# Kernel optimization log

Measured on AMD Instinct MI355X. Metric: run time of the kernel, lower is better.

Reference implementation:

```python
import jax, jax.numpy as jnp
import numpy as np

N_NODES = 50000
N_EDGES = 800000
IN_DIM, HID_DIM, OUT_DIM = 128, 128, 64


def setup_inputs() -> dict:
    key = jax.random.key(0)
    ks = jax.random.split(key, 8)
    x = jax.random.normal(ks[0], (N_NODES, IN_DIM), dtype=jnp.float32)
    edge_index = jax.random.randint(ks[1], (2, N_EDGES), 0, N_NODES, dtype=jnp.int64)
    # GCNConv uses Glorot weights + zero bias; any random init is fine for a reference
    W1 = jax.random.normal(ks[2], (IN_DIM, HID_DIM), dtype=jnp.float32) / np.sqrt(IN_DIM)
    b1 = jnp.zeros((HID_DIM,), dtype=jnp.float32)
    W2 = jax.random.normal(ks[3], (HID_DIM, OUT_DIM), dtype=jnp.float32) / np.sqrt(HID_DIM)
    b2 = jnp.zeros((OUT_DIM,), dtype=jnp.float32)
    Wfc = jax.random.normal(ks[4], (OUT_DIM, 2), dtype=jnp.float32) / np.sqrt(OUT_DIM)
    bfc = jnp.zeros((2,), dtype=jnp.float32)
    return {"x": x, "edge_index": edge_index, "W1": W1, "b1": b1,
            "W2": W2, "b2": b2, "Wfc": Wfc, "bfc": bfc}


def _gcn_conv(x, src, dst, W, b, n_nodes):
    """PyG GCNConv: out = D^{-1/2} (A+I) D^{-1/2} (x W) + b."""
    xw = x @ W  # [N, F_out] transform before propagation
    ones = jnp.ones(src.shape[0], dtype=xw.dtype)
    deg = jax.ops.segment_sum(ones, dst, num_segments=n_nodes) + 1.0  # +1 for self-loop
    dinv = jax.lax.rsqrt(deg)
    norm = dinv[src] * dinv[dst]  # [E]
    msg = xw[src] * norm[:, None]  # gather + scale: [E, F_out]
    agg = jax.ops.segment_sum(msg, dst, num_segments=n_nodes)  # scatter-add
    agg = agg + xw * (dinv * dinv)[:, None]  # self-loop contribution (norm = 1/deg)
    return agg + b


def reference(x, edge_index, W1, b1, W2, b2, Wfc, bfc):
    n = x.shape[0]
    src, dst = edge_index[0], edge_index[1]
    h = jax.nn.relu(_gcn_conv(x, src, dst, W1, b1, n))
    # dropout is identity in eval mode
    h = _gcn_conv(h, src, dst, W2, b2, n)
    h = h @ Wfc + bfc
    return jax.nn.leaky_relu(h, negative_slope=0.01)
```

## Files before the change

kernel.cpp:

```cpp
#include <hip/hip_runtime.h>
#include <hip/hip_fp16.h>

#define IN_DIM 128
#define HID_DIM 128
#define OUT_DIM 64
#define BINW 128
#define BINSHIFT 7
#define MAXBIN 512
#define CAP 4096
#define CNTSTRIDE 16
#define SC_GRID 256
#define SBUF 3456

typedef _Float16 f16x8 __attribute__((ext_vector_type(8)));
typedef float f32x4 __attribute__((ext_vector_type(4)));

__global__ __launch_bounds__(256) void k_build_gemm(const float* __restrict__ x,
                                                    const float* __restrict__ W,
                                                    __half* __restrict__ xwh,
                                                    const int* __restrict__ src,
                                                    const int* __restrict__ dst,
                                                    int* __restrict__ bin_cnt,
                                                    int* __restrict__ ovf_cnt,
                                                    unsigned int* __restrict__ ovf,
                                                    unsigned int* __restrict__ ebin,
                                                    int N, int E, int nbin) {
    __shared__ union SMem {
        unsigned int wt_raw[8192];
        struct {
            int h[MAXBIN];
            int excl[MAXBIN];
            int base_s[MAXBIN];
            int ps[256];
            unsigned int sortbuf[SBUF];
        } sc;
    } smem;
    const int nGemm = (N + 127) >> 7;
    int tid = threadIdx.x;

    if ((int)blockIdx.x < nGemm) {
        char* wb = (char*)smem.wt_raw;
        {
            int kk0 = (tid & 15) * 2;
            int c8  = (tid >> 4) * 8;
#pragma unroll
            for (int i = 0; i < 4; ++i) {
                int kk = i * 32 + kk0;
                const float* w0 = W + (size_t)kk * HID_DIM + c8;
                const float* w1 = w0 + HID_DIM;
                float4 a0 = *(const float4*)w0;
                float4 a1 = *(const float4*)(w0 + 4);
                float4 b0 = *(const float4*)w1;
                float4 b1 = *(const float4*)(w1 + 4);
                float va[8] = {a0.x, a0.y, a0.z, a0.w, a1.x, a1.y, a1.z, a1.w};
                float vb[8] = {b0.x, b0.y, b0.z, b0.w, b1.x, b1.y, b1.z, b1.w};
#pragma unroll
                for (int j = 0; j < 8; ++j) {
                    int col = c8 + j;
                    int byte = (col << 8) + (kk << 1);
                    byte ^= ((col & 7) << 4);
                    *(__half2*)(wb + byte) = __floats2half2_rn(va[j], vb[j]);
                }
            }
        }
        int lane = tid & 63;
        int wv   = tid >> 6;
        int lcol = lane & 15;
        int lk   = (lane >> 4) << 3;
        int swz  = (lcol & 7) << 4;
        int rb   = blockIdx.x * 128 + wv * 32;
        int rows[2];
        const float* xp[2];
#pragma unroll
        for (int r = 0; r < 2; ++r) {
            int row = rb + 16 * r + lcol;
            rows[r] = row;
            if (row > N - 1) row = N - 1;
            xp[r] = x + (size_t)row * IN_DIM + lk;
        }
        f32x4 acc[2][8];
#pragma unroll
        for (int r = 0; r < 2; ++r)
#pragma unroll
            for (int c = 0; c < 8; ++c) acc[r][c] = (f32x4){0.f, 0.f, 0.f, 0.f};

        __syncthreads();

        auto mk = [](float4 f0, float4 f1, f16x8& hi, f16x8& lo) {
            float f[8] = {f0.x, f0.y, f0.z, f0.w, f1.x, f1.y, f1.z, f1.w};
#pragma unroll
            for (int e = 0; e < 8; ++e) {
                _Float16 h = (_Float16)f[e];
                hi[e] = h;
                lo[e] = (_Float16)(f[e] - (float)h);
            }
        };
#pragma unroll
        for (int kc = 0; kc < 4; ++kc) {
            f16x8 xhi[2], xlo[2];
#pragma unroll
            for (int r = 0; r < 2; ++r) {
                float4 f0 = *(const float4*)(xp[r] + kc * 32);
                float4 f1 = *(const float4*)(xp[r] + kc * 32 + 4);
                mk(f0, f1, xhi[r], xlo[r]);
            }
#pragma unroll
            for (int c = 0; c < 8; ++c) {
                int ad = ((c << 12) | (lcol << 8) | ((kc << 6) + (lk << 1))) ^ swz;
                f16x8 wfrag = *(const f16x8*)(wb + ad);
                acc[0][c] = __builtin_amdgcn_mfma_f32_16x16x32_f16(wfrag, xhi[0], acc[0][c], 0, 0, 0);
                acc[0][c] = __builtin_amdgcn_mfma_f32_16x16x32_f16(wfrag, xlo[0], acc[0][c], 0, 0, 0);
                acc[1][c] = __builtin_amdgcn_mfma_f32_16x16x32_f16(wfrag, xhi[1], acc[1][c], 0, 0, 0);
                acc[1][c] = __builtin_amdgcn_mfma_f32_16x16x32_f16(wfrag, xlo[1], acc[1][c], 0, 0, 0);
            }
        }
        int cq = lane >> 4;
#pragma unroll
        for (int r = 0; r < 2; ++r) {
            if (rows[r] < N) {
                uint2* p = (uint2*)(xwh + (size_t)rows[r] * HID_DIM);
#pragma unroll
                for (int c = 0; c < 8; ++c) {
                    union { __half2 h[2]; uint2 u; } pk;
                    pk.h[0] = __floats2half2_rn(acc[r][c].x, acc[r][c].y);
                    pk.h[1] = __floats2half2_rn(acc[r][c].z, acc[r][c].w);
                    p[4 * c + cq] = pk.u;
                }
            }
        }
    } else {
        int sb = blockIdx.x - nGemm;
        int* h = smem.sc.h;
        int* excl = smem.sc.excl;
        int* base_s = smem.sc.base_s;
        int* ps = smem.sc.ps;
        unsigned int* sortbuf = smem.sc.sortbuf;
        for (int k = tid; k < MAXBIN; k += 256) h[k] = 0;
        __syncthreads();
        int per = E / SC_GRID;
        int ebeg = sb * per;
        int eend = (sb + 1 == SC_GRID) ? E : ebeg + per;
        for (int i = ebeg + tid; i < eend; i += 256)
            atomicAdd(&h[dst[i] >> BINSHIFT], 1);
        __syncthreads();
        int b0 = 2 * tid, b1 = 2 * tid + 1;
        int c0 = h[b0], c1 = h[b1];
        ps[tid] = c0 + c1;
        __syncthreads();
        for (int off = 1; off < 256; off <<= 1) {
            int v = (tid >= off) ? ps[tid - off] : 0;
            __syncthreads();
            ps[tid] += v;
            __syncthreads();
        }
        int Pprev = (tid > 0) ? ps[tid - 1] : 0;
        excl[b0] = Pprev;
        excl[b1] = Pprev + c0;
        __syncthreads();
        for (int k = tid; k < nbin; k += 256) {
            int c = h[k];
            base_s[k] = (c > 0) ? atomicAdd(&bin_cnt[k * CNTSTRIDE], c) : 0;
            h[k] = 0;
        }
        __syncthreads();
        for (int i = ebeg + tid; i < eend; i += 256) {
            unsigned int s = (unsigned int)src[i];
            unsigned int d = (unsigned int)dst[i];
            int b = (int)(d >> BINSHIFT);
            int r = atomicAdd(&h[b], 1);
            sortbuf[excl[b] + r] = s | (d << 16);
        }
        __syncthreads();
        int tot = eend - ebeg;
        for (int i = tid; i < tot; i += 256) {
            unsigned int p = sortbuf[i];
            int b = (int)(p >> (16 + BINSHIFT));
            int g = base_s[b] + (i - excl[b]);
            if (g < CAP) ebin[(size_t)b * CAP + g] = p;
            else ovf[atomicAdd(ovf_cnt, 1)] = p;
        }
    }
}

__global__ __launch_bounds__(256) void k_fill(const unsigned int* __restrict__ ebin,
                                              const int* __restrict__ bin_cnt,
                                              const int* __restrict__ ovf_cnt,
                                              const unsigned int* __restrict__ ovf,
                                              int* __restrict__ row_ptr,
                                              unsigned short* __restrict__ degu,
                                              unsigned short* __restrict__ csr_src,
                                              float* __restrict__ dinv,
                                              const float* __restrict__ W2,
                                              const float* __restrict__ Wfc,
                                              const float* __restrict__ b2,
                                              const float* __restrict__ bfc,
                                              float* __restrict__ Wc,
                                              float* __restrict__ bc,
                                              int N, int nbin) {
    __shared__ int cnt[BINW];
    __shared__ int excl[BINW];
    __shared__ int start[BINW];
    int k = blockIdx.x;
    int node0 = k * BINW;
    int nn = min(BINW, N - node0);
    int t = threadIdx.x;
    if (t < BINW) cnt[t] = 0;
    __syncthreads();
    int cnt_k = min(bin_cnt[k * CNTSTRIDE], CAP);
    const unsigned int* seg = ebin + (size_t)k * CAP;
    for (int i = t; i < cnt_k; i += 256)
        atomicAdd(&cnt[(seg[i] >> 16) & (BINW - 1)], 1);
    int novf = *ovf_cnt;
    for (int i = t; i < novf; i += 256) {
        unsigned int e = ovf[i];
        if ((int)(e >> (16 + BINSHIFT)) == k)
            atomicAdd(&cnt[(e >> 16) & (BINW - 1)], 1);
    }
    __syncthreads();
    if (t < BINW) excl[t] = (t < nn) ? cnt[t] : 0;
    __syncthreads();
    for (int off = 1; off < BINW; off <<= 1) {
        int u = 0;
        if (t < BINW && t >= off) u = excl[t - off];
        __syncthreads();
        if (t < BINW) excl[t] += u;
        __syncthreads();
    }
    if (t < nn) {
        int deg = cnt[t];
        int e0 = k * CAP + excl[t] - deg;
        start[t] = e0;
        row_ptr[node0 + t] = e0;
        degu[node0 + t] = (unsigned short)deg;
        dinv[node0 + t] = rsqrtf((float)deg + 1.0f);
        cnt[t] = 0;
    }
    __syncthreads();
    for (int i = t; i < cnt_k; i += 256) {
        unsigned int e = seg[i];
        int dl = (e >> 16) & (BINW - 1);
        int slot = start[dl] + atomicAdd(&cnt[dl], 1);
        csr_src[slot] = (unsigned short)(e & 0xffffu);
    }
    for (int i = t; i < novf; i += 256) {
        unsigned int e = ovf[i];
        if ((int)(e >> (16 + BINSHIFT)) == k) {
            int dl = (e >> 16) & (BINW - 1);
            int slot = start[dl] + atomicAdd(&cnt[dl], 1);
            csr_src[slot] = (unsigned short)(e & 0xffffu);
        }
    }
    if (k == 0) {
        int kk = t >> 1, j = t & 1;
        float acc = 0.f;
#pragma unroll 8
        for (int m = 0; m < OUT_DIM; ++m) acc += W2[kk * OUT_DIM + m] * Wfc[m * 2 + j];
        Wc[kk * 2 + j] = acc;
        if (kk == 0) {
            float b = 0.f;
#pragma unroll 8
            for (int m = 0; m < OUT_DIM; ++m) b += b2[m] * Wfc[m * 2 + j];
            bc[j] = b + bfc[j];
        }
    }
}

__global__ __launch_bounds__(256) void k_agg1z(const int* __restrict__ row_ptr,
                                               const unsigned short* __restrict__ degu,
                                               const unsigned short* __restrict__ csr_src,
                                               const float* __restrict__ dinv,
                                               const __half* __restrict__ xwh,
                                               const float* __restrict__ b1,
                                               const float* __restrict__ Wc,
                                               float* __restrict__ z, int N) {
    constexpr int F = HID_DIM;
    constexpr int L = F / 8;
    constexpr int EPW = 64 / L;
    __shared__ float Wcs[HID_DIM * 2];
    int tid = threadIdx.x;
    if (tid < 64) ((float4*)Wcs)[tid] = ((const float4*)Wc)[tid];
    __syncthreads();
    int node = (blockIdx.x * 256 + tid) >> 6;
    if (node >= N) return;
    int lane = tid & 63;
    int sub = lane / L;
    int c   = lane % L;
    int beg = row_ptr[node];
    int end = beg + degu[node];
    float dd = dinv[node];
    uint4 us = *(const uint4*)(xwh + (size_t)node * F + c * 8);
    float4 b1a = *(const float4*)(b1 + c * 8);
    float4 b1b = *(const float4*)(b1 + c * 8 + 4);
    float a0 = 0.f, a1 = 0.f, a2 = 0.f, a3 = 0.f;
    float a4 = 0.f, a5 = 0.f, a6 = 0.f, a7 = 0.f;
    auto acc = [&](uint4 u, float w) {
        float2 v0 = __half22float2(*(__half2*)&u.x);
        float2 v1 = __half22float2(*(__half2*)&u.y);
        float2 v2 = __half22float2(*(__half2*)&u.z);
        float2 v3 = __half22float2(*(__half2*)&u.w);
        a0 = fmaf(v0.x, w, a0); a1 = fmaf(v0.y, w, a1);
        a2 = fmaf(v1.x, w, a2); a3 = fmaf(v1.y, w, a3);
        a4 = fmaf(v2.x, w, a4); a5 = fmaf(v2.y, w, a5);
        a6 = fmaf(v3.x, w, a6); a7 = fmaf(v3.y, w, a7);
    };
    int j = beg + sub;
    for (; j + 3 * EPW < end; j += 4 * EPW) {
        int s0 = csr_src[j];
        int s1 = csr_src[j + EPW];
        int s2 = csr_src[j + 2 * EPW];
        int s3 = csr_src[j + 3 * EPW];
        uint4 u0 = *(const uint4*)(xwh + (size_t)s0 * F + c * 8);
        uint4 u1 = *(const uint4*)(xwh + (size_t)s1 * F + c * 8);
        uint4 u2 = *(const uint4*)(xwh + (size_t)s2 * F + c * 8);
        uint4 u3 = *(const uint4*)(xwh + (size_t)s3 * F + c * 8);
        float w0 = dinv[s0];
        float w1 = dinv[s1];
        float w2 = dinv[s2];
        float w3 = dinv[s3];
        acc(u0, w0); acc(u1, w1); acc(u2, w2); acc(u3, w3);
    }
    for (; j < end; j += EPW) {
        int s = csr_src[j];
        uint4 u = *(const uint4*)(xwh + (size_t)s * F + c * 8);
        acc(u, dinv[s]);
    }
#pragma unroll
    for (int off = L; off < 64; off <<= 1) {
        a0 += __shfl_xor(a0, off); a1 += __shfl_xor(a1, off);
        a2 += __shfl_xor(a2, off); a3 += __shfl_xor(a3, off);
        a4 += __shfl_xor(a4, off); a5 += __shfl_xor(a5, off);
        a6 += __shfl_xor(a6, off); a7 += __shfl_xor(a7, off);
    }
    float2 v0 = __half22float2(*(__half2*)&us.x);
    float2 v1 = __half22float2(*(__half2*)&us.y);
    float2 v2 = __half22float2(*(__half2*)&us.z);
    float2 v3 = __half22float2(*(__half2*)&us.w);
    float h[8];
    h[0] = fmaxf(fmaf(fmaf(v0.x, dd, a0), dd, b1a.x), 0.f);
    h[1] = fmaxf(fmaf(fmaf(v0.y, dd, a1), dd, b1a.y), 0.f);
    h[2] = fmaxf(fmaf(fmaf(v1.x, dd, a2), dd, b1a.z), 0.f);
    h[3] = fmaxf(fmaf(fmaf(v1.y, dd, a3), dd, b1a.w), 0.f);
    h[4] = fmaxf(fmaf(fmaf(v2.x, dd, a4), dd, b1b.x), 0.f);
    h[5] = fmaxf(fmaf(fmaf(v2.y, dd, a5), dd, b1b.y), 0.f);
    h[6] = fmaxf(fmaf(fmaf(v3.x, dd, a6), dd, b1b.z), 0.f);
    h[7] = fmaxf(fmaf(fmaf(v3.y, dd, a7), dd, b1b.w), 0.f);
    float o0 = 0.f, o1 = 0.f;
#pragma unroll
    for (int k = 0; k < 8; ++k) {
        o0 += h[k] * Wcs[(c * 8 + k) * 2 + 0];
        o1 += h[k] * Wcs[(c * 8 + k) * 2 + 1];
    }
#pragma unroll
    for (int off = 1; off < L; off <<= 1) {
        o0 += __shfl_xor(o0, off);
        o1 += __shfl_xor(o1, off);
    }
    if (lane == 0) {
        float2 r; r.x = o0 * dd; r.y = o1 * dd;
        *(float2*)(z + (size_t)node * 2) = r;
    }
}

__global__ __launch_bounds__(256) void k_agg2(const int* __restrict__ row_ptr,
                                              const unsigned short* __restrict__ degu,
                                              const unsigned short* __restrict__ csr_src,
                                              const float* __restrict__ dinv,
                                              const float* __restrict__ z,
                                              const float* __restrict__ bc,
                                              float* __restrict__ out, int N) {
    int tid = threadIdx.x;
    int gwave = (blockIdx.x * 256 + tid) >> 6;
    int lane = tid & 63;
    int grp = lane >> 3, li = lane & 7;
    int node = gwave * 8 + grp;
    if (node >= N) return;
    int beg = row_ptr[node];
    int end = beg + degu[node];
    float s0 = 0.f, s1 = 0.f;
    int j = beg + li;
    for (; j + 8 < end; j += 16) {
        int sa = csr_src[j];
        int sb = csr_src[j + 8];
        float2 za = *(const float2*)(z + (size_t)sa * 2);
        float2 zb = *(const float2*)(z + (size_t)sb * 2);
        s0 += za.x + zb.x; s1 += za.y + zb.y;
    }
    if (j < end) {
        int s = csr_src[j];
        float2 zv = *(const float2*)(z + (size_t)s * 2);
        s0 += zv.x; s1 += zv.y;
    }
#pragma unroll
    for (int off = 1; off < 8; off <<= 1) {
        s0 += __shfl_xor(s0, off);
        s1 += __shfl_xor(s1, off);
    }
    if (li == 0) {
        float2 zs = *(const float2*)(z + (size_t)node * 2);
        float dd = dinv[node];
        float o0 = (s0 + zs.x) * dd + bc[0];
        float o1 = (s1 + zs.y) * dd + bc[1];
        float2 r;
        r.x = o0 > 0.f ? o0 : 0.01f * o0;
        r.y = o1 > 0.f ? o1 : 0.01f * o1;
        *(float2*)(out + (size_t)node * 2) = r;
    }
}

extern "C" void kernel_launch(void* const* d_in, const int* in_sizes, int n_in,
                              void* d_out, int out_size, void* d_ws, size_t ws_size,
                              hipStream_t stream) {
    const float* x   = (const float*)d_in[0];
    const int*   ei  = (const int*)d_in[1];
    const float* W1  = (const float*)d_in[2];
    const float* b1  = (const float*)d_in[3];
    const float* W2  = (const float*)d_in[4];
    const float* b2  = (const float*)d_in[5];
    const float* Wfc = (const float*)d_in[6];
    const float* bfc = (const float*)d_in[7];

    const int N = in_sizes[0] / IN_DIM;
    const int E = in_sizes[1] / 2;
    const int* src = ei;
    const int* dst = ei + E;
    const int nbin = (N + BINW - 1) / BINW;

    char* base = (char*)d_ws;
    size_t off = 0;
    auto take = [&](size_t bytes) { size_t o = off; off = (off + bytes + 255) & ~(size_t)255; return (void*)(base + o); };
    int*    row_ptr  = (int*)take((size_t)N * 4);
    unsigned short* degu = (unsigned short*)take((size_t)N * 2);
    unsigned short* csr_src = (unsigned short*)take((size_t)nbin * CAP * 2);
    int*    bin_cnt  = (int*)take((size_t)(nbin * CNTSTRIDE + CNTSTRIDE) * 4);
    int*    ovf_cnt  = bin_cnt + nbin * CNTSTRIDE;
    unsigned int* ovf = (unsigned int*)take((size_t)E * 4);
    unsigned int* ebin = (unsigned int*)take((size_t)nbin * CAP * 4);
    float*  dinv     = (float*)take((size_t)N * 4);
    __half* xw1h     = (__half*)take((size_t)N * HID_DIM * 2);
    float*  zbuf     = (float*)take((size_t)N * 2 * 4);
    float*  Wc       = (float*)take((size_t)HID_DIM * 2 * 4);
    float*  bc       = (float*)take(2 * 4);

    hipMemsetAsync(bin_cnt, 0, (size_t)(nbin * CNTSTRIDE + CNTSTRIDE) * 4, stream);

    const int nGemm = (N + 127) / 128;
    k_build_gemm<<<nGemm + SC_GRID, 256, 0, stream>>>(x, W1, xw1h, src, dst, bin_cnt,
                                                      ovf_cnt, ovf, ebin, N, E, nbin);
    k_fill<<<nbin, 256, 0, stream>>>(ebin, bin_cnt, ovf_cnt, ovf, row_ptr, degu,
                                     csr_src, dinv, W2, Wfc, b2, bfc, Wc, bc, N, nbin);
    k_agg1z<<<(N + 3) / 4, 256, 0, stream>>>(row_ptr, degu, csr_src, dinv, xw1h, b1, Wc, zbuf, N);
    const int nAgg2 = ((N + 7) / 8 * 64 + 255) / 256;
    k_agg2<<<nAgg2, 256, 0, stream>>>(row_ptr, degu, csr_src, dinv, zbuf, bc, (float*)d_out, N);
}
```

Measured before the change: 154.6 us.

## Split XW1 into feature chunks mapped to XCDs and atomically reduce z

The GEMM now writes the fp16 XW1 output in four column-chunk planes of 32 features each. Layer-1 aggregation maps each chunk to a pair of XCDs by block index, so each XCD's L2 only has to cache one quarter of the feature table during the random gathers. Partial z projections from each chunk are combined with float atomics, and k_fill zero-initialises z for this. Two smaller changes ride along: the binning pass stages edges in shared memory so src/dst are read once, and k_fill caches its bin segment in LDS. The cost is extra atomics, a reliance on round-robin block-to-XCD placement, and a larger LDS footprint.

```diff
diff --git a/kernel.cpp b/kernel.cpp
--- a/kernel.cpp
+++ b/kernel.cpp
@@ -11,6 +11,7 @@
 #define CNTSTRIDE 16
 #define SC_GRID 256
 #define SBUF 3456
+#define NCHUNK 4
 
 typedef _Float16 f16x8 __attribute__((ext_vector_type(8)));
 typedef float f32x4 __attribute__((ext_vector_type(4)));
@@ -32,7 +33,8 @@
             int excl[MAXBIN];
             int base_s[MAXBIN];
             int ps[256];
-            unsigned int sortbuf[SBUF];
+            unsigned int sb1[SBUF];
+            unsigned int sb2[SBUF];
         } sc;
     } smem;
     const int nGemm = (N + 127) >> 7;
@@ -115,16 +117,17 @@
             }
         }
         int cq = lane >> 4;
+        const size_t chstride = (size_t)N * 32;
 #pragma unroll
         for (int r = 0; r < 2; ++r) {
             if (rows[r] < N) {
-                uint2* p = (uint2*)(xwh + (size_t)rows[r] * HID_DIM);
+                __half* rowp = xwh + (size_t)rows[r] * 32;
 #pragma unroll
                 for (int c = 0; c < 8; ++c) {
                     union { __half2 h[2]; uint2 u; } pk;
                     pk.h[0] = __floats2half2_rn(acc[r][c].x, acc[r][c].y);
                     pk.h[1] = __floats2half2_rn(acc[r][c].z, acc[r][c].w);
-                    p[4 * c + cq] = pk.u;
+                    *(uint2*)(rowp + (size_t)(c >> 1) * chstride + 16 * (c & 1) + 4 * cq) = pk.u;
                 }
             }
         }
@@ -134,14 +137,19 @@
         int* excl = smem.sc.excl;
         int* base_s = smem.sc.base_s;
         int* ps = smem.sc.ps;
-        unsigned int* sortbuf = smem.sc.sortbuf;
+        unsigned int* sb1 = smem.sc.sb1;
+        unsigned int* sb2 = smem.sc.sb2;
         for (int k = tid; k < MAXBIN; k += 256) h[k] = 0;
         __syncthreads();
         int per = E / SC_GRID;
         int ebeg = sb * per;
         int eend = (sb + 1 == SC_GRID) ? E : ebeg + per;
-        for (int i = ebeg + tid; i < eend; i += 256)
-            atomicAdd(&h[dst[i] >> BINSHIFT], 1);
+        for (int i = ebeg + tid; i < eend; i += 256) {
+            unsigned int s = (unsigned int)src[i];
+            unsigned int d = (unsigned int)dst[i];
+            sb1[i - ebeg] = s | (d << 16);
+            atomicAdd(&h[d >> BINSHIFT], 1);
+        }
         __syncthreads();
         int b0 = 2 * tid, b1 = 2 * tid + 1;
         int c0 = h[b0], c1 = h[b1];
@@ -163,17 +171,16 @@
             h[k] = 0;
         }
         __syncthreads();
-        for (int i = ebeg + tid; i < eend; i += 256) {
-            unsigned int s = (unsigned int)src[i];
-            unsigned int d = (unsigned int)dst[i];
-            int b = (int)(d >> BINSHIFT);
-            int r = atomicAdd(&h[b], 1);
-            sortbuf[excl[b] + r] = s | (d << 16);
-        }
-        __syncthreads();
         int tot = eend - ebeg;
         for (int i = tid; i < tot; i += 256) {
-            unsigned int p = sortbuf[i];
+            unsigned int p = sb1[i];
+            int b = (int)(p >> (16 + BINSHIFT));
+            int r = atomicAdd(&h[b], 1);
+            sb2[excl[b] + r] = p;
+        }
+        __syncthreads();
+        for (int i = tid; i < tot; i += 256) {
+            unsigned int p = sb2[i];
             int b = (int)(p >> (16 + BINSHIFT));
             int g = base_s[b] + (i - excl[b]);
             if (g < CAP) ebin[(size_t)b * CAP + g] = p;
@@ -196,20 +203,24 @@
                                               const float* __restrict__ bfc,
                                               float* __restrict__ Wc,
                                               float* __restrict__ bc,
+                                              float* __restrict__ z,
                                               int N, int nbin) {
     __shared__ int cnt[BINW];
     __shared__ int excl[BINW];
     __shared__ int start[BINW];
+    __shared__ unsigned int segl[CAP];
     int k = blockIdx.x;
     int node0 = k * BINW;
     int nn = min(BINW, N - node0);
     int t = threadIdx.x;
     if (t < BINW) cnt[t] = 0;
-    __syncthreads();
     int cnt_k = min(bin_cnt[k * CNTSTRIDE], CAP);
     const unsigned int* seg = ebin + (size_t)k * CAP;
+    for (int i = t; i < cnt_k; i += 256) segl[i] = seg[i];
+    if (t < nn) *(float2*)(z + 2 * (node0 + t)) = make_float2(0.f, 0.f);
+    __syncthreads();
     for (int i = t; i < cnt_k; i += 256)
-        atomicAdd(&cnt[(seg[i] >> 16) & (BINW - 1)], 1);
+        atomicAdd(&cnt[(segl[i] >> 16) & (BINW - 1)], 1);
     int novf = *ovf_cnt;
     for (int i = t; i < novf; i += 256) {
         unsigned int e = ovf[i];
@@ -237,7 +248,7 @@
     }
     __syncthreads();
     for (int i = t; i < cnt_k; i += 256) {
-        unsigned int e = seg[i];
+        unsigned int e = segl[i];
         int dl = (e >> 16) & (BINW - 1);
         int slot = start[dl] + atomicAdd(&cnt[dl], 1);
         csr_src[slot] = (unsigned short)(e & 0xffffu);
@@ -269,31 +280,32 @@
                                                const unsigned short* __restrict__ degu,
                                                const unsigned short* __restrict__ csr_src,
                                                const float* __restrict__ dinv,
-                                               const __half* __restrict__ xwh,
+                                               const __half* __restrict__ xwc,
                                                const float* __restrict__ b1,
                                                const float* __restrict__ Wc,
-                                               float* __restrict__ z, int N) {
-    constexpr int F = HID_DIM;
-    constexpr int L = F / 8;
-    constexpr int EPW = 64 / L;
-    __shared__ float Wcs[HID_DIM * 2];
+                                               float* __restrict__ z, int N, int halfB) {
     int tid = threadIdx.x;
-    if (tid < 64) ((float4*)Wcs)[tid] = ((const float4*)Wc)[tid];
-    __syncthreads();
-    int node = (blockIdx.x * 256 + tid) >> 6;
-    if (node >= N) return;
+    int bid = blockIdx.x;
+    int xcd = bid & 7;
+    int jb  = bid >> 3;
+    int chunk = xcd >> 1;
+    int nodeblk = jb + (xcd & 1) * halfB;
+    int wv = tid >> 6;
     int lane = tid & 63;
-    int sub = lane / L;
-    int c   = lane % L;
-    int beg = row_ptr[node];
-    int end = beg + degu[node];
-    float dd = dinv[node];
-    uint4 us = *(const uint4*)(xwh + (size_t)node * F + c * 8);
-    float4 b1a = *(const float4*)(b1 + c * 8);
-    float4 b1b = *(const float4*)(b1 + c * 8 + 4);
+    int grp = lane >> 4;
+    int l16 = lane & 15;
+    int sub = l16 >> 2;
+    int li  = l16 & 3;
+    int node = nodeblk * 16 + wv * 4 + grp;
+    int nd = node < N ? node : N - 1;
+    const __half* xc = xwc + (size_t)chunk * N * 32;
+    int beg = row_ptr[nd];
+    int end = beg + degu[nd];
+    float dd = dinv[nd];
+    uint4 us = *(const uint4*)(xc + (size_t)nd * 32 + li * 8);
     float a0 = 0.f, a1 = 0.f, a2 = 0.f, a3 = 0.f;
     float a4 = 0.f, a5 = 0.f, a6 = 0.f, a7 = 0.f;
-    auto acc = [&](uint4 u, float w) {
+    auto accf = [&](uint4 u, float w) {
         float2 v0 = __half22float2(*(__half2*)&u.x);
         float2 v1 = __half22float2(*(__half2*)&u.y);
         float2 v2 = __half22float2(*(__half2*)&u.z);
@@ -303,29 +315,24 @@
         a4 = fmaf(v2.x, w, a4); a5 = fmaf(v2.y, w, a5);
         a6 = fmaf(v3.x, w, a6); a7 = fmaf(v3.y, w, a7);
     };
-    int j = beg + sub;
-    for (; j + 3 * EPW < end; j += 4 * EPW) {
-        int s0 = csr_src[j];
-        int s1 = csr_src[j + EPW];
-        int s2 = csr_src[j + 2 * EPW];
-        int s3 = csr_src[j + 3 * EPW];
-        uint4 u0 = *(const uint4*)(xwh + (size_t)s0 * F + c * 8);
-        uint4 u1 = *(const uint4*)(xwh + (size_t)s1 * F + c * 8);
-        uint4 u2 = *(const uint4*)(xwh + (size_t)s2 * F + c * 8);
-        uint4 u3 = *(const uint4*)(xwh + (size_t)s3 * F + c * 8);
+    int jj = beg + sub;
+    for (; jj + 4 < end; jj += 8) {
+        int s0 = csr_src[jj];
+        int s1 = csr_src[jj + 4];
         float w0 = dinv[s0];
         float w1 = dinv[s1];
-        float w2 = dinv[s2];
-        float w3 = dinv[s3];
-        acc(u0, w0); acc(u1, w1); acc(u2, w2); acc(u3, w3);
-    }
-    for (; j < end; j += EPW) {
-        int s = csr_src[j];
-        uint4 u = *(const uint4*)(xwh + (size_t)s * F + c * 8);
-        acc(u, dinv[s]);
-    }
-#pragma unroll
-    for (int off = L; off < 64; off <<= 1) {
+        uint4 u0 = *(const uint4*)(xc + (size_t)s0 * 32 + li * 8);
+        uint4 u1 = *(const uint4*)(xc + (size_t)s1 * 32 + li * 8);
+        accf(u0, w0); accf(u1, w1);
+    }
+    if (jj < end) {
+        int s0 = csr_src[jj];
+        float w0 = dinv[s0];
+        uint4 u0 = *(const uint4*)(xc + (size_t)s0 * 32 + li * 8);
+        accf(u0, w0);
+    }
+#pragma unroll
+    for (int off = 4; off < 16; off <<= 1) {
         a0 += __shfl_xor(a0, off); a1 += __shfl_xor(a1, off);
         a2 += __shfl_xor(a2, off); a3 += __shfl_xor(a3, off);
         a4 += __shfl_xor(a4, off); a5 += __shfl_xor(a5, off);
@@ -335,29 +342,31 @@
     float2 v1 = __half22float2(*(__half2*)&us.y);
     float2 v2 = __half22float2(*(__half2*)&us.z);
     float2 v3 = __half22float2(*(__half2*)&us.w);
-    float h[8];
-    h[0] = fmaxf(fmaf(fmaf(v0.x, dd, a0), dd, b1a.x), 0.f);
-    h[1] = fmaxf(fmaf(fmaf(v0.y, dd, a1), dd, b1a.y), 0.f);
-    h[2] = fmaxf(fmaf(fmaf(v1.x, dd, a2), dd, b1a.z), 0.f);
-    h[3] = fmaxf(fmaf(fmaf(v1.y, dd, a3), dd, b1a.w), 0.f);
-    h[4] = fmaxf(fmaf(fmaf(v2.x, dd, a4), dd, b1b.x), 0.f);
-    h[5] = fmaxf(fmaf(fmaf(v2.y, dd, a5), dd, b1b.y), 0.f);
-    h[6] = fmaxf(fmaf(fmaf(v3.x, dd, a6), dd, b1b.z), 0.f);
-    h[7] = fmaxf(fmaf(fmaf(v3.y, dd, a7), dd, b1b.w), 0.f);
-    float o0 = 0.f, o1 = 0.f;
-#pragma unroll
-    for (int k = 0; k < 8; ++k) {
-        o0 += h[k] * Wcs[(c * 8 + k) * 2 + 0];
-        o1 += h[k] * Wcs[(c * 8 + k) * 2 + 1];
-    }
-#pragma unroll
-    for (int off = 1; off < L; off <<= 1) {
-        o0 += __shfl_xor(o0, off);
-        o1 += __shfl_xor(o1, off);
-    }
-    if (lane == 0) {
-        float2 r; r.x = o0 * dd; r.y = o1 * dd;
-        *(float2*)(z + (size_t)node * 2) = r;
+    int cbase = chunk * 32 + li * 8;
+    float4 b1a = *(const float4*)(b1 + cbase);
+    float4 b1b = *(const float4*)(b1 + cbase + 4);
+    float h0 = fmaxf(fmaf(fmaf(v0.x, dd, a0), dd, b1a.x), 0.f);
+    float h1 = fmaxf(fmaf(fmaf(v0.y, dd, a1), dd, b1a.y), 0.f);
+    float h2 = fmaxf(fmaf(fmaf(v1.x, dd, a2), dd, b1a.z), 0.f);
+    float h3 = fmaxf(fmaf(fmaf(v1.y, dd, a3), dd, b1a.w), 0.f);
+    float h4 = fmaxf(fmaf(fmaf(v2.x, dd, a4), dd, b1b.x), 0.f);
+    float h5 = fmaxf(fmaf(fmaf(v2.y, dd, a5), dd, b1b.y), 0.f);
+    float h6 = fmaxf(fmaf(fmaf(v3.x, dd, a6), dd, b1b.z), 0.f);
+    float h7 = fmaxf(fmaf(fmaf(v3.y, dd, a7), dd, b1b.w), 0.f);
+    const float* wp = Wc + cbase * 2;
+    float4 w0 = *(const float4*)wp;
+    float4 w1 = *(const float4*)(wp + 4);
+    float4 w2 = *(const float4*)(wp + 8);
+    float4 w3 = *(const float4*)(wp + 12);
+    float o0 = h0 * w0.x + h1 * w0.z + h2 * w1.x + h3 * w1.z
+             + h4 * w2.x + h5 * w2.z + h6 * w3.x + h7 * w3.z;
+    float o1 = h0 * w0.y + h1 * w0.w + h2 * w1.y + h3 * w1.w
+             + h4 * w2.y + h5 * w2.w + h6 * w3.y + h7 * w3.w;
+    o0 += __shfl_xor(o0, 1); o0 += __shfl_xor(o0, 2);
+    o1 += __shfl_xor(o1, 1); o1 += __shfl_xor(o1, 2);
+    if (l16 == 0 && node < N) {
+        atomicAdd(&z[2 * node],     o0 * dd);
+        atomicAdd(&z[2 * node + 1], o1 * dd);
     }
 }
 
@@ -447,8 +456,10 @@
     k_build_gemm<<<nGemm + SC_GRID, 256, 0, stream>>>(x, W1, xw1h, src, dst, bin_cnt,
                                                       ovf_cnt, ovf, ebin, N, E, nbin);
     k_fill<<<nbin, 256, 0, stream>>>(ebin, bin_cnt, ovf_cnt, ovf, row_ptr, degu,
-                                     csr_src, dinv, W2, Wfc, b2, bfc, Wc, bc, N, nbin);
-    k_agg1z<<<(N + 3) / 4, 256, 0, stream>>>(row_ptr, degu, csr_src, dinv, xw1h, b1, Wc, zbuf, N);
+                                     csr_src, dinv, W2, Wfc, b2, bfc, Wc, bc, zbuf, N, nbin);
+    const int nbChunk = (N + 15) / 16;
+    const int halfB = (nbChunk + 1) / 2;
+    k_agg1z<<<8 * halfB, 256, 0, stream>>>(row_ptr, degu, csr_src, dinv, xw1h, b1, Wc, zbuf, N, halfB);
     const int nAgg2 = ((N + 7) / 8 * 64 + 255) / 256;
     k_agg2<<<nAgg2, 256, 0, stream>>>(row_ptr, degu, csr_src, dinv, zbuf, bc, (float*)d_out, N);
 }
```

New measurement: 163.4 us. 5.7% more time.
